# Kernel optimization log

Hardware: AMD Instinct MI355X
Metric: run time of the kernel (lower is better)

## Reference

```python
import jax, jax.numpy as jnp
import numpy as np

FP8_MAX = 448.0  # max finite value of float8_e4m3fn
F8 = jnp.float8_e4m3fn


def _quantize_fp8(v):
    # Saturating round-to-nearest FP8 E4M3 quantization (torch .to(float8_e4m3fn) saturates)
    return jnp.clip(v, -FP8_MAX, FP8_MAX).astype(F8).astype(jnp.float32)


def setup_inputs() -> dict:
    key = jax.random.key(0)
    k1, k2, k3 = jax.random.split(key, 3)
    M, K, N = 8192, 4096, 4096
    x = jax.random.normal(k1, (M, K), dtype=jnp.float16)
    # Build a realistic quantized weight: fp32 master weight -> per-tensor scale -> fp8 values
    w = jax.random.normal(k2, (N, K), dtype=jnp.float32) * 0.02
    weight_scale = jnp.reshape(jnp.maximum(jnp.max(jnp.abs(w)) / FP8_MAX, 1e-12), (1,))
    weight_quantized = _quantize_fp8(w / weight_scale[0])  # stored as fp32 holding exact fp8 values
    bias = (jax.random.normal(k3, (N,), dtype=jnp.float32) * 0.01).astype(jnp.float16)
    return {"x": x, "weight_quantized": weight_quantized, "weight_scale": weight_scale, "bias": bias}


def reference(x, weight_quantized, weight_scale, bias):
    # _kernel_forward: dynamic per-tensor input scale from abs-max reduction
    input_absmax = jnp.maximum(jnp.max(jnp.abs(x)).astype(jnp.float32), 1e-12)
    scale_a = input_absmax / FP8_MAX
    # NOTE: faithful to source — x is cast to fp8 directly (NOT divided by scale first)
    x_fp8 = _quantize_fp8(x.astype(jnp.float32))  # [M, K]
    scale_b = weight_scale[0]  # numel()==1 branch
    acc = jnp.matmul(x_fp8, weight_quantized.T)  # [M, N], fp32 accumulate
    out = acc * (scale_a * scale_b) + bias.astype(jnp.float32)
    return out.astype(jnp.float16)
```

## Files before the change

kernel.cpp:

```cpp
#include <hip/hip_runtime.h>
#include <hip/hip_bf16.h>
#include <stdint.h>

#define M_DIM 8192
#define N_DIM 4096
#define K_DIM 4096
#define FP8MAX 448.0f
#define CANARY 0x5CA1AB1Eu

typedef float floatx4 __attribute__((ext_vector_type(4)));
typedef float floatx16 __attribute__((ext_vector_type(16)));
typedef short short8 __attribute__((ext_vector_type(8)));
typedef int int8v __attribute__((ext_vector_type(8)));

__device__ __forceinline__ unsigned int f2bfbits(float f) {
    union { float f; unsigned int u; } v; v.f = f;
    return (v.u + 0x7fffu + ((v.u >> 16) & 1u)) >> 16;
}

__device__ __forceinline__ uint2 quant4(float a, float b, float c, float d) {
    int p8 = __builtin_amdgcn_cvt_pk_fp8_f32(a, b, 0, false);
    p8 = __builtin_amdgcn_cvt_pk_fp8_f32(c, d, p8, true);
    float qa = __builtin_amdgcn_cvt_f32_fp8(p8, 0);
    float qb = __builtin_amdgcn_cvt_f32_fp8(p8, 1);
    float qc = __builtin_amdgcn_cvt_f32_fp8(p8, 2);
    float qd = __builtin_amdgcn_cvt_f32_fp8(p8, 3);
    return make_uint2(f2bfbits(qa) | (f2bfbits(qb) << 16),
                      f2bfbits(qc) | (f2bfbits(qd) << 16));
}

__device__ __forceinline__ unsigned int quant4_fp8(float a, float b, float c, float d) {
    int p8 = __builtin_amdgcn_cvt_pk_fp8_f32(a, b, 0, false);
    p8 = __builtin_amdgcn_cvt_pk_fp8_f32(c, d, p8, true);
    return (unsigned int)p8;
}


__global__ __launch_bounds__(256) void quant_x_ws8(const uint4* __restrict__ x,
                                                   unsigned int* __restrict__ xq,
                                                   float* __restrict__ partials) {
    const int tid = blockIdx.x * 256 + threadIdx.x;
    float vmax = 0.f;
    for (int c = tid; c < (M_DIM * K_DIM) / 4; c += 2048 * 256) {
        uint4 v = x[c];
        float a = __uint_as_float(v.x), b = __uint_as_float(v.y);
        float cc = __uint_as_float(v.z), d = __uint_as_float(v.w);
        vmax = fmaxf(vmax, fmaxf(fmaxf(fabsf(a), fabsf(b)), fmaxf(fabsf(cc), fabsf(d))));
        xq[c] = quant4_fp8(a, b, cc, d);
    }
    #pragma unroll
    for (int off = 32; off >= 1; off >>= 1)
        vmax = fmaxf(vmax, __shfl_xor(vmax, off, 64));
    __shared__ float smax[4];
    if ((threadIdx.x & 63) == 0) smax[threadIdx.x >> 6] = vmax;
    __syncthreads();
    if (threadIdx.x == 0)
        partials[blockIdx.x] = fmaxf(fmaxf(smax[0], smax[1]), fmaxf(smax[2], smax[3]));
}

__global__ __launch_bounds__(256) void quant_w_ws8(const uint4* __restrict__ w,
                                                   unsigned int* __restrict__ wq) {
    const int tid = blockIdx.x * 256 + threadIdx.x;
    for (int c = tid; c < (N_DIM * K_DIM) / 4; c += 1024 * 256) {
        uint4 v = w[c];
        wq[c] = quant4_fp8(__uint_as_float(v.x), __uint_as_float(v.y),
                           __uint_as_float(v.z), __uint_as_float(v.w));
    }
}

__global__ __launch_bounds__(256) void scale_ws(const float* __restrict__ partials,
                                                const float* __restrict__ wscale,
                                                float* __restrict__ scb) {
    float vmax = 0.f;
    for (int i = threadIdx.x; i < 2048; i += 256) vmax = fmaxf(vmax, partials[i]);
    #pragma unroll
    for (int off = 32; off >= 1; off >>= 1)
        vmax = fmaxf(vmax, __shfl_xor(vmax, off, 64));
    __shared__ float smax[4];
    if ((threadIdx.x & 63) == 0) smax[threadIdx.x >> 6] = vmax;
    __syncthreads();
    if (threadIdx.x == 0) {
        float m = fmaxf(fmaxf(smax[0], smax[1]), fmaxf(smax[2], smax[3]));
        scb[0] = (fmaxf(m, 1e-12f) / FP8MAX) * wscale[0];
        ((unsigned int*)scb)[1] = CANARY;
    }
}

__device__ __forceinline__ int8v pack8(uint4 u0, uint4 u1) {
    int8v r;
    r[0] = (int)u0.x; r[1] = (int)u0.y; r[2] = (int)u0.z; r[3] = (int)u0.w;
    r[4] = (int)u1.x; r[5] = (int)u1.y; r[6] = (int)u1.z; r[7] = (int)u1.w;
    return r;
}

__global__ __launch_bounds__(256, 2) void gemm_fp8_kernel(
    const unsigned char* __restrict__ Aq,
    const unsigned char* __restrict__ Bq,
    const unsigned char* __restrict__ scb,
    const float* __restrict__ bias,
    float* __restrict__ out) {
    __shared__ __align__(16) unsigned char lds[2 * 128 * 128];
    const int tid = threadIdx.x;
    const int l = tid & 63, wv = tid >> 6, wm = wv >> 1, wn = wv & 1;
    const int bm = blockIdx.y, bn = blockIdx.x;
    const int r = tid >> 1, kq = (tid & 1) * 64;

    const float scl = *(const float*)scb;
    const unsigned int canary = *(const unsigned int*)(scb + 4);

    const unsigned char* gA = Aq + (size_t)(bm * 128 + r) * 4096 + kq;
    const unsigned char* gB = Bq + (size_t)(bn * 128 + r) * 4096 + kq;
    const int swzW = (r & 7) << 4;
    unsigned char* sA = lds + r * 128;
    unsigned char* sB = lds + 16384 + r * 128;

    const int swzR = (l & 7) << 4;
    int aBase[2], bBase[2], rdOff[2][2][2];
    #pragma unroll
    for (int i = 0; i < 2; ++i) {
        aBase[i] = (wm * 64 + i * 32 + (l & 31)) * 128;
        bBase[i] = 16384 + (wn * 64 + i * 32 + (l & 31)) * 128;
        #pragma unroll
        for (int s = 0; s < 2; ++s) {
            int off = s * 64 + (l >> 5) * 32;
            rdOff[i][s][0] = (off) ^ swzR;
            rdOff[i][s][1] = (off + 16) ^ swzR;
        }
    }

    floatx16 acc[2][2];
    #pragma unroll
    for (int i = 0; i < 2; ++i)
        #pragma unroll
        for (int j = 0; j < 2; ++j)
            acc[i][j] = (floatx16)0.f;

    for (int kt = 0; kt < K_DIM / 128; ++kt) {
        uint4 a0 = *(const uint4*)(gA);
        uint4 a1 = *(const uint4*)(gA + 16);
        uint4 a2 = *(const uint4*)(gA + 32);
        uint4 a3 = *(const uint4*)(gA + 48);
        uint4 b0 = *(const uint4*)(gB);
        uint4 b1 = *(const uint4*)(gB + 16);
        uint4 b2 = *(const uint4*)(gB + 32);
        uint4 b3 = *(const uint4*)(gB + 48);
        gA += 128;
        gB += 128;
        __syncthreads();
        *(uint4*)(sA + (((kq +  0) ^ swzW))) = a0;
        *(uint4*)(sA + (((kq + 16) ^ swzW))) = a1;
        *(uint4*)(sA + (((kq + 32) ^ swzW))) = a2;
        *(uint4*)(sA + (((kq + 48) ^ swzW))) = a3;
        *(uint4*)(sB + (((kq +  0) ^ swzW))) = b0;
        *(uint4*)(sB + (((kq + 16) ^ swzW))) = b1;
        *(uint4*)(sB + (((kq + 32) ^ swzW))) = b2;
        *(uint4*)(sB + (((kq + 48) ^ swzW))) = b3;
        __syncthreads();

        int8v af[2][2], bf[2][2];
        #pragma unroll
        for (int i = 0; i < 2; ++i) {
            #pragma unroll
            for (int s = 0; s < 2; ++s) {
                uint4 u0 = *(const uint4*)(lds + aBase[i] + rdOff[i][s][0]);
                uint4 u1 = *(const uint4*)(lds + aBase[i] + rdOff[i][s][1]);
                af[i][s] = pack8(u0, u1);
                uint4 v0 = *(const uint4*)(lds + bBase[i] + rdOff[i][s][0]);
                uint4 v1 = *(const uint4*)(lds + bBase[i] + rdOff[i][s][1]);
                bf[i][s] = pack8(v0, v1);
            }
        }
        #pragma unroll
        for (int s = 0; s < 2; ++s)
            #pragma unroll
            for (int i = 0; i < 2; ++i)
                #pragma unroll
                for (int j = 0; j < 2; ++j)
                    acc[i][j] = __builtin_amdgcn_mfma_scale_f32_32x32x64_f8f6f4(
                        af[i][s], bf[j][s], acc[i][j],
                        0 , 0 ,
                        0, 0x7F,
                        0, 0x7F);
    }

    float marker = 0.f;
    if (canary != CANARY) marker = 222.f;
    else if (scl != scl || fabsf(scl) > 1e-1f) marker = 1000.f;
    else if (fabsf(scl) > 1e-4f) marker = 777.f;
    else if (fabsf(scl) < 1e-8f) marker = 333.f;

    float bj[2];
    #pragma unroll
    for (int j = 0; j < 2; ++j)
        bj[j] = bias[bn * 128 + wn * 64 + j * 32 + (l & 31)];

    #pragma unroll
    for (int i = 0; i < 2; ++i) {
        #pragma unroll
        for (int rg = 0; rg < 4; ++rg) {
            #pragma unroll
            for (int rr = 0; rr < 4; ++rr) {
                int row = bm * 128 + wm * 64 + i * 32 + rg * 8 + rr + 4 * (l >> 5);
                float* orow = out + (size_t)row * N_DIM;
                #pragma unroll
                for (int j = 0; j < 2; ++j) {
                    int col = bn * 128 + wn * 64 + j * 32 + (l & 31);
                    float v = acc[i][j][rg * 4 + rr] * scl + bj[j];
                    if (marker != 0.f) v = marker;
                    else if (bj[j] != bj[j]) v = 111.f;
                    else if (v != v) v = 555.f;
                    orow[col] = v;
                }
            }
        }
    }
}


__global__ __launch_bounds__(256) void quant_w_kernel(unsigned char* wbuf) {
    const size_t t = (size_t)blockIdx.x * 256 + threadIdx.x;
    uint4* p = (uint4*)(wbuf + t * 256);
    uint4 r[16];
    #pragma unroll
    for (int i = 0; i < 16; ++i) r[i] = p[i];
    const float* f = (const float*)r;
    unsigned int o[32];
    #pragma unroll
    for (int i = 0; i < 16; ++i) {
        unsigned int b0 = f2bfbits(f[4 * i + 0]);
        unsigned int b1 = f2bfbits(f[4 * i + 1]);
        unsigned int b2 = f2bfbits(f[4 * i + 2]);
        unsigned int b3 = f2bfbits(f[4 * i + 3]);
        ((uint2*)o)[i] = make_uint2(b0 | (b1 << 16), b2 | (b3 << 16));
    }
    uint4* q = (uint4*)(wbuf + t * 256);
    #pragma unroll
    for (int i = 0; i < 8; ++i) q[i] = ((uint4*)o)[i];
}

__global__ __launch_bounds__(256) void quant_x_kernel(unsigned char* xbuf, unsigned char* wbuf) {
    const size_t t = (size_t)blockIdx.x * 256 + threadIdx.x;
    uint4* p = (uint4*)(xbuf + t * 256);
    uint4 r[16];
    #pragma unroll
    for (int i = 0; i < 16; ++i) r[i] = p[i];
    const float* f = (const float*)r;
    float vmax = 0.f;
    unsigned int o[32];
    #pragma unroll
    for (int i = 0; i < 16; ++i) {
        float a = f[4 * i + 0], b = f[4 * i + 1], c = f[4 * i + 2], d = f[4 * i + 3];
        vmax = fmaxf(vmax, fmaxf(fmaxf(fabsf(a), fabsf(b)), fmaxf(fabsf(c), fabsf(d))));
        ((uint2*)o)[i] = quant4(a, b, c, d);
    }
    uint4* q = (uint4*)(xbuf + t * 256);
    #pragma unroll
    for (int i = 0; i < 8; ++i) q[i] = ((uint4*)o)[i];
    #pragma unroll
    for (int off = 32; off >= 1; off >>= 1)
        vmax = fmaxf(vmax, __shfl_xor(vmax, off, 64));
    __shared__ float smax[4];
    if ((threadIdx.x & 63) == 0) smax[threadIdx.x >> 6] = vmax;
    __syncthreads();
    if (threadIdx.x == 0)
        *(float*)(wbuf + ((size_t)blockIdx.x + 1) * 256 + 128) =
            fmaxf(fmaxf(smax[0], smax[1]), fmaxf(smax[2], smax[3]));
}

__global__ __launch_bounds__(256) void scale_kernel(unsigned char* wbuf, const float* wscale) {
    float vmax = 0.f;
    for (int i = threadIdx.x; i < 2048; i += 256)
        vmax = fmaxf(vmax, *(const float*)(wbuf + ((size_t)i + 1) * 256 + 128));
    #pragma unroll
    for (int off = 32; off >= 1; off >>= 1)
        vmax = fmaxf(vmax, __shfl_xor(vmax, off, 64));
    __shared__ float smax[4];
    if ((threadIdx.x & 63) == 0) smax[threadIdx.x >> 6] = vmax;
    __syncthreads();
    if (threadIdx.x == 0) {
        float m = fmaxf(fmaxf(smax[0], smax[1]), fmaxf(smax[2], smax[3]));
        *(float*)(wbuf + 128) = (fmaxf(m, 1e-12f) / FP8MAX) * wscale[0];
        *(unsigned int*)(wbuf + 132) = CANARY;
    }
}

__global__ __launch_bounds__(256, 2) void gemm_bf16_kernel(
    const unsigned char* __restrict__ Aq,
    const unsigned char* __restrict__ Bq,
    int rs, int ktb,
    const unsigned char* __restrict__ scb,
    const float* __restrict__ bias,
    float* __restrict__ out) {
    __shared__ __align__(16) short lds[2 * 128 * 72];
    const int tid = threadIdx.x;
    const int l = tid & 63, wv = tid >> 6, wm = wv >> 1, wn = wv & 1;
    const int bm = blockIdx.y, bn = blockIdx.x;
    const int r = tid >> 1, kq = (tid & 1) * 64;

    const float scl = *(const float*)scb;
    const unsigned int canary = *(const unsigned int*)(scb + 4);

    const unsigned char* gA = Aq + (size_t)(bm * 128 + r) * rs + kq;
    const unsigned char* gB = Bq + (size_t)(bn * 128 + r) * rs + kq;
    short* sA = lds + r * 72 + kq / 2;
    short* sB = lds + 9216 + r * 72 + kq / 2;

    int aOff[4][2], bOff[4][2];
    #pragma unroll
    for (int i = 0; i < 4; ++i) {
        #pragma unroll
        for (int s = 0; s < 2; ++s) {
            int rowa = wm * 64 + i * 16 + (l & 15);
            aOff[i][s] = rowa * 72 + s * 32 + (l >> 4) * 8;
            int rowb = wn * 64 + i * 16 + (l & 15);
            bOff[i][s] = 9216 + rowb * 72 + s * 32 + (l >> 4) * 8;
        }
    }

    floatx4 acc[4][4];
    #pragma unroll
    for (int i = 0; i < 4; ++i)
        #pragma unroll
        for (int j = 0; j < 4; ++j)
            acc[i][j] = (floatx4)0.f;

    for (int kt = 0; kt < K_DIM / 64; ++kt) {
        uint4 a0 = *(const uint4*)(gA);
        uint4 a1 = *(const uint4*)(gA + 16);
        uint4 a2 = *(const uint4*)(gA + 32);
        uint4 a3 = *(const uint4*)(gA + 48);
        uint4 b0 = *(const uint4*)(gB);
        uint4 b1 = *(const uint4*)(gB + 16);
        uint4 b2 = *(const uint4*)(gB + 32);
        uint4 b3 = *(const uint4*)(gB + 48);
        gA += ktb;
        gB += ktb;
        __syncthreads();
        *(uint4*)(sA +  0) = a0;  *(uint4*)(sA +  8) = a1;
        *(uint4*)(sA + 16) = a2;  *(uint4*)(sA + 24) = a3;
        *(uint4*)(sB +  0) = b0;  *(uint4*)(sB +  8) = b1;
        *(uint4*)(sB + 16) = b2;  *(uint4*)(sB + 24) = b3;
        __syncthreads();

        short8 af[4][2], bf[4][2];
        #pragma unroll
        for (int i = 0; i < 4; ++i) {
            af[i][0] = *(const short8*)(lds + aOff[i][0]);
            af[i][1] = *(const short8*)(lds + aOff[i][1]);
            bf[i][0] = *(const short8*)(lds + bOff[i][0]);
            bf[i][1] = *(const short8*)(lds + bOff[i][1]);
        }
        #pragma unroll
        for (int s = 0; s < 2; ++s)
            #pragma unroll
            for (int i = 0; i < 4; ++i)
                #pragma unroll
                for (int j = 0; j < 4; ++j)
                    acc[i][j] = __builtin_amdgcn_mfma_f32_16x16x32_bf16(
                        af[i][s], bf[j][s], acc[i][j], 0, 0, 0);
    }

    float marker = 0.f;
    if (canary != CANARY) marker = 222.f;
    else if (scl != scl || fabsf(scl) > 1e-1f) marker = 1000.f;
    else if (fabsf(scl) > 1e-4f) marker = 777.f;
    else if (fabsf(scl) < 1e-8f) marker = 333.f;

    float bj[4];
    #pragma unroll
    for (int j = 0; j < 4; ++j) {
        int col = bn * 128 + wn * 64 + j * 16 + (l & 15);
        bj[j] = bias[col];
    }
    #pragma unroll
    for (int i = 0; i < 4; ++i) {
        #pragma unroll
        for (int rr = 0; rr < 4; ++rr) {
            int row = bm * 128 + wm * 64 + i * 16 + (l >> 4) * 4 + rr;
            float* orow = out + (size_t)row * N_DIM;
            #pragma unroll
            for (int j = 0; j < 4; ++j) {
                int col = bn * 128 + wn * 64 + j * 16 + (l & 15);
                float v = acc[i][j][rr] * scl + bj[j];
                if (marker != 0.f) v = marker;
                else if (bj[j] != bj[j]) v = 111.f;
                else if (v != v) v = 555.f;
                orow[col] = v;
            }
        }
    }
}

extern "C" void kernel_launch(void* const* d_in, const int* in_sizes, int n_in,
                              void* d_out, int out_size, void* d_ws, size_t ws_size,
                              hipStream_t stream) {
    unsigned char* x = (unsigned char*)d_in[0];
    unsigned char* w = (unsigned char*)d_in[1];
    const float* wscale = (const float*)d_in[2];
    const float* bias = (const float*)d_in[3];
    float* out = (float*)d_out;

    const size_t XQ8 = (size_t)M_DIM * K_DIM;
    const size_t WQ8 = (size_t)N_DIM * K_DIM;
    unsigned char* ws = (unsigned char*)d_ws;

    if (ws_size >= XQ8 + WQ8 + 2048 * 4 + 64) {
        unsigned char* xq = ws;
        unsigned char* wq = ws + XQ8;
        float* partials = (float*)(ws + XQ8 + WQ8);
        unsigned char* scb = ws + XQ8 + WQ8 + 8192;
        quant_w_ws8<<<1024, 256, 0, stream>>>((const uint4*)w, (unsigned int*)wq);
        quant_x_ws8<<<2048, 256, 0, stream>>>((const uint4*)x, (unsigned int*)xq, partials);
        scale_ws<<<1, 256, 0, stream>>>(partials, wscale, (float*)scb);
        gemm_fp8_kernel<<<dim3(N_DIM / 128, M_DIM / 128), 256, 0, stream>>>(
            xq, wq, scb, bias, out);
    } else {
        quant_w_kernel<<<1024, 256, 0, stream>>>(w);
        quant_x_kernel<<<2048, 256, 0, stream>>>(x, w);
        scale_kernel<<<1, 256, 0, stream>>>(w, wscale);
        gemm_bf16_kernel<<<dim3(N_DIM / 128, M_DIM / 128), 256, 0, stream>>>(
            x, w, 16384, 256, w + 128, bias, out);
    }
}
```

Baseline: 417.2 us.

## Fuse x/w quantization into one kernel and fold scale reduction into GEMM

Merges the separate weight-quantize, input-quantize and scale-reduction launches into a single quantization kernel split by block index. Each thread now handles 16 elements and writes 16-byte packed outputs instead of 4-byte ones. The final abs-max reduction over the 2048 partials moves into the GEMM epilogue, where every block redundantly re-reduces them. This removes two launches and their serialization gaps, at the cost of extra reads and two barriers per GEMM block.

```diff
diff --git a/kernel.cpp b/kernel.cpp
--- a/kernel.cpp
+++ b/kernel.cpp
@@ -29,60 +29,49 @@
                       f2bfbits(qc) | (f2bfbits(qd) << 16));
 }
 
-__device__ __forceinline__ unsigned int quant4_fp8(float a, float b, float c, float d) {
-    int p8 = __builtin_amdgcn_cvt_pk_fp8_f32(a, b, 0, false);
-    p8 = __builtin_amdgcn_cvt_pk_fp8_f32(c, d, p8, true);
+__device__ __forceinline__ unsigned int q4(uint4 v) {
+    int p8 = __builtin_amdgcn_cvt_pk_fp8_f32(__uint_as_float(v.x), __uint_as_float(v.y), 0, false);
+    p8 = __builtin_amdgcn_cvt_pk_fp8_f32(__uint_as_float(v.z), __uint_as_float(v.w), p8, true);
     return (unsigned int)p8;
 }
 
-
-__global__ __launch_bounds__(256) void quant_x_ws8(const uint4* __restrict__ x,
-                                                   unsigned int* __restrict__ xq,
+__device__ __forceinline__ float amax4(uint4 v, float m) {
+    float a = fabsf(__uint_as_float(v.x)), b = fabsf(__uint_as_float(v.y));
+    float c = fabsf(__uint_as_float(v.z)), d = fabsf(__uint_as_float(v.w));
+    return fmaxf(m, fmaxf(fmaxf(a, b), fmaxf(c, d)));
+}
+
+__global__ __launch_bounds__(256) void quant_fused(const uint4* __restrict__ x,
+                                                   const uint4* __restrict__ w,
+                                                   uint4* __restrict__ xq,
+                                                   uint4* __restrict__ wq,
                                                    float* __restrict__ partials) {
-    const int tid = blockIdx.x * 256 + threadIdx.x;
-    float vmax = 0.f;
-    for (int c = tid; c < (M_DIM * K_DIM) / 4; c += 2048 * 256) {
-        uint4 v = x[c];
-        float a = __uint_as_float(v.x), b = __uint_as_float(v.y);
-        float cc = __uint_as_float(v.z), d = __uint_as_float(v.w);
-        vmax = fmaxf(vmax, fmaxf(fmaxf(fabsf(a), fabsf(b)), fmaxf(fabsf(cc), fabsf(d))));
-        xq[c] = quant4_fp8(a, b, cc, d);
-    }
-    #pragma unroll
-    for (int off = 32; off >= 1; off >>= 1)
-        vmax = fmaxf(vmax, __shfl_xor(vmax, off, 64));
-    __shared__ float smax[4];
-    if ((threadIdx.x & 63) == 0) smax[threadIdx.x >> 6] = vmax;
-    __syncthreads();
-    if (threadIdx.x == 0)
-        partials[blockIdx.x] = fmaxf(fmaxf(smax[0], smax[1]), fmaxf(smax[2], smax[3]));
-}
-
-__global__ __launch_bounds__(256) void quant_w_ws8(const uint4* __restrict__ w,
-                                                   unsigned int* __restrict__ wq) {
-    const int tid = blockIdx.x * 256 + threadIdx.x;
-    for (int c = tid; c < (N_DIM * K_DIM) / 4; c += 1024 * 256) {
-        uint4 v = w[c];
-        wq[c] = quant4_fp8(__uint_as_float(v.x), __uint_as_float(v.y),
-                           __uint_as_float(v.z), __uint_as_float(v.w));
-    }
-}
-
-__global__ __launch_bounds__(256) void scale_ws(const float* __restrict__ partials,
-                                                const float* __restrict__ wscale,
-                                                float* __restrict__ scb) {
-    float vmax = 0.f;
-    for (int i = threadIdx.x; i < 2048; i += 256) vmax = fmaxf(vmax, partials[i]);
-    #pragma unroll
-    for (int off = 32; off >= 1; off >>= 1)
-        vmax = fmaxf(vmax, __shfl_xor(vmax, off, 64));
-    __shared__ float smax[4];
-    if ((threadIdx.x & 63) == 0) smax[threadIdx.x >> 6] = vmax;
-    __syncthreads();
-    if (threadIdx.x == 0) {
-        float m = fmaxf(fmaxf(smax[0], smax[1]), fmaxf(smax[2], smax[3]));
-        scb[0] = (fmaxf(m, 1e-12f) / FP8MAX) * wscale[0];
-        ((unsigned int*)scb)[1] = CANARY;
+    if (blockIdx.x < 1024) {
+        const int tid = blockIdx.x * 256 + threadIdx.x;
+        for (int c = tid; c < (N_DIM * K_DIM) / 16; c += 1024 * 256) {
+            uint4 v0 = w[4 * c + 0], v1 = w[4 * c + 1];
+            uint4 v2 = w[4 * c + 2], v3 = w[4 * c + 3];
+            wq[c] = make_uint4(q4(v0), q4(v1), q4(v2), q4(v3));
+        }
+    } else {
+        const int b = blockIdx.x - 1024;
+        const int tid = b * 256 + threadIdx.x;
+        float vmax = 0.f;
+        for (int c = tid; c < (M_DIM * K_DIM) / 16; c += 2048 * 256) {
+            uint4 v0 = x[4 * c + 0], v1 = x[4 * c + 1];
+            uint4 v2 = x[4 * c + 2], v3 = x[4 * c + 3];
+            vmax = amax4(v0, vmax); vmax = amax4(v1, vmax);
+            vmax = amax4(v2, vmax); vmax = amax4(v3, vmax);
+            xq[c] = make_uint4(q4(v0), q4(v1), q4(v2), q4(v3));
+        }
+        #pragma unroll
+        for (int off = 32; off >= 1; off >>= 1)
+            vmax = fmaxf(vmax, __shfl_xor(vmax, off, 64));
+        __shared__ float smax[4];
+        if ((threadIdx.x & 63) == 0) smax[threadIdx.x >> 6] = vmax;
+        __syncthreads();
+        if (threadIdx.x == 0)
+            partials[b] = fmaxf(fmaxf(smax[0], smax[1]), fmaxf(smax[2], smax[3]));
     }
 }
 
@@ -96,7 +85,8 @@
 __global__ __launch_bounds__(256, 2) void gemm_fp8_kernel(
     const unsigned char* __restrict__ Aq,
     const unsigned char* __restrict__ Bq,
-    const unsigned char* __restrict__ scb,
+    const float* __restrict__ partials,
+    const float* __restrict__ wscale,
     const float* __restrict__ bias,
     float* __restrict__ out) {
     __shared__ __align__(16) unsigned char lds[2 * 128 * 128];
@@ -104,9 +94,6 @@
     const int l = tid & 63, wv = tid >> 6, wm = wv >> 1, wn = wv & 1;
     const int bm = blockIdx.y, bn = blockIdx.x;
     const int r = tid >> 1, kq = (tid & 1) * 64;
-
-    const float scl = *(const float*)scb;
-    const unsigned int canary = *(const unsigned int*)(scb + 4);
 
     const unsigned char* gA = Aq + (size_t)(bm * 128 + r) * 4096 + kq;
     const unsigned char* gB = Bq + (size_t)(bn * 128 + r) * 4096 + kq;
@@ -183,9 +170,24 @@
                         0, 0x7F);
     }
 
+    float pm = 0.f;
+    #pragma unroll
+    for (int i = 0; i < 8; ++i) pm = fmaxf(pm, partials[tid + 256 * i]);
+    #pragma unroll
+    for (int off = 32; off >= 1; off >>= 1)
+        pm = fmaxf(pm, __shfl_xor(pm, off, 64));
+    __shared__ float sred[5];
+    if ((tid & 63) == 0) sred[tid >> 6] = pm;
+    __syncthreads();
+    if (tid == 0) {
+        float m = fmaxf(fmaxf(sred[0], sred[1]), fmaxf(sred[2], sred[3]));
+        sred[4] = (fmaxf(m, 1e-12f) / FP8MAX) * wscale[0];
+    }
+    __syncthreads();
+    const float scl = sred[4];
+
     float marker = 0.f;
-    if (canary != CANARY) marker = 222.f;
-    else if (scl != scl || fabsf(scl) > 1e-1f) marker = 1000.f;
+    if (scl != scl || fabsf(scl) > 1e-1f) marker = 1000.f;
     else if (fabsf(scl) > 1e-4f) marker = 777.f;
     else if (fabsf(scl) < 1e-8f) marker = 333.f;
 
@@ -408,12 +410,10 @@
         unsigned char* xq = ws;
         unsigned char* wq = ws + XQ8;
         float* partials = (float*)(ws + XQ8 + WQ8);
-        unsigned char* scb = ws + XQ8 + WQ8 + 8192;
-        quant_w_ws8<<<1024, 256, 0, stream>>>((const uint4*)w, (unsigned int*)wq);
-        quant_x_ws8<<<2048, 256, 0, stream>>>((const uint4*)x, (unsigned int*)xq, partials);
-        scale_ws<<<1, 256, 0, stream>>>(partials, wscale, (float*)scb);
+        quant_fused<<<3072, 256, 0, stream>>>((const uint4*)x, (const uint4*)w,
+                                              (uint4*)xq, (uint4*)wq, partials);
         gemm_fp8_kernel<<<dim3(N_DIM / 128, M_DIM / 128), 256, 0, stream>>>(
-            xq, wq, scb, bias, out);
+            xq, wq, partials, wscale, bias, out);
     } else {
         quant_w_kernel<<<1024, 256, 0, stream>>>(w);
         quant_x_kernel<<<2048, 256, 0, stream>>>(x, w);
```

Result: no change. 414.5 us (-0.7%).
